# Kernel optimization log

Measured on AMD Instinct MI355X. Metric: run time of the kernel, lower is better.

Reference implementation:

```python
import jax, jax.numpy as jnp
import numpy as np

NUM_WIRES = 12
NUM_LAYERS = 3
BATCH = 8192
DIM = 2 ** NUM_WIRES


def _rx(theta):
    # RX(t) = [[cos(t/2), -i sin(t/2)], [-i sin(t/2), cos(t/2)]]; theta scalar or (B,)
    h = theta * 0.5
    c = jnp.cos(h).astype(jnp.complex64)
    s = (-1j) * jnp.sin(h).astype(jnp.complex64)
    return jnp.stack([jnp.stack([c, s], -1), jnp.stack([s, c], -1)], -2)


def _ry(theta):
    # RY(t) = [[cos(t/2), -sin(t/2)], [sin(t/2), cos(t/2)]]
    h = theta * 0.5
    c = jnp.cos(h)
    s = jnp.sin(h)
    m = jnp.stack([jnp.stack([c, -s], -1), jnp.stack([s, c], -1)], -2)
    return m.astype(jnp.complex64)


def _apply_1q(psi, mat, wire):
    # psi: (B, 2**n); pennylane wire 0 is most significant bit
    B = psi.shape[0]
    s = psi.reshape(B, 2 ** wire, 2, -1)
    if mat.ndim == 2:
        out = jnp.einsum('ij,bajc->baic', mat, s)
    else:  # per-sample gate, mat: (B, 2, 2)
        out = jnp.einsum('bij,bajc->baic', mat, s)
    return out.reshape(B, -1)


def _cnot(psi, control, target):
    B = psi.shape[0]
    a, b = (control, target) if control < target else (target, control)
    s = psi.reshape(B, 2 ** a, 2, 2 ** (b - a - 1), 2, -1)
    if control == a:
        # control on axis 2, flip target (axis 4) where control bit == 1
        s = s.at[:, :, 1].set(s[:, :, 1, :, ::-1])
    else:
        # control on axis 4, flip target (axis 2) where control bit == 1
        s = s.at[:, :, :, :, 1].set(s[:, :, ::-1, :, 1])
    return s.reshape(B, -1)


def _circuit(angles, weights):
    # angles: (B, n) per-sample input rotations; weights: (L, n, 2)
    B = angles.shape[0]
    n = NUM_WIRES
    psi = jnp.zeros((B, DIM), jnp.complex64).at[:, 0].set(1.0)
    for i in range(n):
        psi = _apply_1q(psi, _rx(angles[:, i]), i)
        psi = _apply_1q(psi, _ry(angles[:, i]), i)
    for l in range(NUM_LAYERS):
        for i in range(n):
            psi = _apply_1q(psi, _rx(weights[l, i, 0]), i)
            psi = _apply_1q(psi, _ry(weights[l, i, 1]), i)
        for i in range(n - 1):
            psi = _cnot(psi, i, i + 1)
        psi = _cnot(psi, n - 1, 0)
    probs = (psi.real ** 2 + psi.imag ** 2).reshape((B,) + (2,) * n)
    zs = []
    for i in range(n):
        other = tuple(j + 1 for j in range(n) if j != i)
        p = probs.sum(other)  # (B, 2)
        zs.append(p[:, 0] - p[:, 1])  # <Z_i> = P(0) - P(1)
    return jnp.stack(zs, -1)  # (B, n)


def setup_inputs() -> dict:
    key = jax.random.key(0)
    ks = jax.random.split(key, 5)
    return {
        'state_real': jax.random.normal(ks[0], (BATCH, DIM), jnp.float32),
        'state_imag': jax.random.normal(ks[1], (BATCH, DIM), jnp.float32),
        'weights': jax.random.normal(ks[2], (NUM_LAYERS, NUM_WIRES, 2), jnp.float32),
        'head_w': jax.random.normal(ks[3], (1, NUM_WIRES), jnp.float32) / np.sqrt(NUM_WIRES).astype(np.float32),
        'head_b': jax.random.normal(ks[4], (1,), jnp.float32),
    }


def reference(state_real, state_imag, weights, head_w, head_b):
    angles = jnp.arctan2(state_imag[:, :NUM_WIRES], state_real[:, :NUM_WIRES])  # (B, n)
    q = _circuit(angles, weights)  # (B, n)
    return (q @ head_w.T + head_b).squeeze(-1)  # (B,)
```

## Files before the change

### kernel.cpp

```cpp
#include <hip/hip_runtime.h>

typedef __fp16 h2v __attribute__((ext_vector_type(2)));
typedef _Float16 f16x8 __attribute__((ext_vector_type(8)));
typedef float f32x4 __attribute__((ext_vector_type(4)));

#define BLK 256
#define BATCH 8192

struct M12 { unsigned r[12]; };

constexpr M12 mp_matrix() {
  M12 m{};
  for (int p = 0; p <= 10; ++p) m.r[p] = (0xFFFu >> p) << p;
  m.r[11] = 0x7FFu;
  return m;
}
constexpr M12 MP = mp_matrix();

constexpr unsigned mv(const M12 m, unsigned v) {
  unsigned y = 0;
  for (int p = 0; p < 12; ++p)
    y |= (unsigned)(__builtin_popcount(m.r[p] & v) & 1) << p;
  return y;
}
constexpr M12 mmul(const M12 a, const M12 b) {
  M12 c{};
  for (int p = 0; p < 12; ++p) {
    unsigned acc = 0;
    for (int q = 0; q < 12; ++q)
      if ((a.r[p] >> q) & 1u) acc ^= b.r[q];
    c.r[p] = acc;
  }
  return c;
}
constexpr M12 minv(const M12 a0) {
  unsigned a[12] = {}, v[12] = {};
  for (int i = 0; i < 12; ++i) { a[i] = a0.r[i]; v[i] = 1u << i; }
  for (int c = 0; c < 12; ++c) {
    int piv = c;
    while (!((a[piv] >> c) & 1u)) ++piv;
    unsigned ta = a[piv], tv = v[piv];
    a[piv] = a[c]; v[piv] = v[c]; a[c] = ta; v[c] = tv;
    for (int r2 = 0; r2 < 12; ++r2)
      if (r2 != c && ((a[r2] >> c) & 1u)) { a[r2] ^= a[c]; v[r2] ^= v[c]; }
  }
  M12 out{};
  for (int i = 0; i < 12; ++i) out.r[i] = v[i];
  return out;
}
constexpr unsigned colq(const M12 m, int q) {
  unsigned c = 0;
  for (int p = 0; p < 12; ++p) c |= ((m.r[p] >> q) & 1u) << p;
  return c;
}
constexpr M12 from_cols(const unsigned (&c)[12]) {
  M12 m{};
  for (int p = 0; p < 12; ++p) {
    unsigned row = 0;
    for (int j = 0; j < 12; ++j) row |= ((c[j] >> p) & 1u) << j;
    m.r[p] = row;
  }
  return m;
}
constexpr M12 mk_id() { M12 m{}; for (int p = 0; p < 12; ++p) m.r[p] = 1u << p; return m; }
constexpr M12 MID = mk_id();
constexpr M12 MPI = minv(MP);

constexpr bool meq(const M12 a, const M12 b) {
  for (int p = 0; p < 12; ++p) if (a.r[p] != b.r[p]) return false;
  return true;
}
static_assert(meq(mmul(MP, MPI), MID), "P inverse");

struct Frame { M12 A, Ai; };
constexpr Frame FID{MID, MID};
constexpr Frame absorb(const Frame f) { return Frame{ mmul(MP, f.A), mmul(f.Ai, MPI) }; }
constexpr Frame apply_tau(const Frame f, const M12 t) {
  return Frame{ mmul(f.A, minv(t)), mmul(t, f.Ai) };
}

struct BSw { unsigned mk[7]; };
constexpr unsigned bswap(const BSw& b, unsigned v) {
  unsigned o = v;
  for (int k = 0; k < 7; ++k)
    if ((v >> (5 + k)) & 1u) o ^= b.mk[k];
  return o;
}
constexpr int rank5(const unsigned* v, int n) {
  unsigned basis[5] = {};
  int r = 0;
  for (int i = 0; i < n; ++i) {
    unsigned x = v[i];
    for (int b = 4; b >= 0; --b) {
      if (!((x >> b) & 1u)) continue;
      if (basis[b]) x ^= basis[b];
      else { basis[b] = x; ++r; break; }
    }
  }
  return r;
}
constexpr int readrank(const BSw& b) {
  unsigned v[5] = { bswap(b, 16u) & 0x1Cu, bswap(b, 32u) & 0x1Cu,
                    bswap(b, 64u) & 0x1Cu, bswap(b, 128u) & 0x1Cu,
                    bswap(b, 8u) & 0x1Cu };
  return rank5(v, 5);
}
constexpr int wrankf(const BSw& b, const unsigned* tv) {
  unsigned v[6] = {};
  for (int k = 0; k < 6; ++k) v[k] = bswap(b, tv[k]) & 0x1Fu;
  return rank5(v, 6);
}
constexpr BSw find_bsw(const M12 T, bool dpass) {
  unsigned src[6] = {16u, 32u, 64u, 128u, dpass ? 4u : 256u, dpass ? 8u : 512u};
  unsigned tv[6] = {};
  for (int k = 0; k < 6; ++k) tv[k] = mv(T, src[k]);
  BSw b{};
  b.mk[0] = 4u;
  int bw = wrankf(b, tv);
  for (int s = 0; s < 2; ++s)
    for (int k = 0; k < 7; ++k) {
      unsigned bestv = b.mk[k];
      for (unsigned v = 0; v < 8; ++v) {
        b.mk[k] = v << 2;
        if (readrank(b) < 3) continue;
        const int wr = wrankf(b, tv);
        if (wr > bw) { bw = wr; bestv = v << 2; }
      }
      b.mk[k] = bestv;
    }
  return b;
}

constexpr M12 mtw_c(const Frame f, const int* qs, const unsigned* tg, int c) {
  unsigned S[12] = {}, D[12] = {}, rows[4] = {};
  for (int i = 0; i < 4; ++i) {
    S[i] = colq(f.Ai, qs[i]);
    D[i] = tg[i];
    rows[i] = f.A.r[qs[i]];
  }
  unsigned R[4] = {rows[0], rows[1], rows[2], rows[3]};
  int pivcol[4] = {-1, -1, -1, -1};
  int nr = 0;
  for (int cc = 0; cc < 12 && nr < 4; ++cc) {
    int pr = -1;
    for (int r2 = nr; r2 < 4; ++r2) if ((R[r2] >> cc) & 1u) { pr = r2; break; }
    if (pr < 0) continue;
    unsigned tmp = R[nr]; R[nr] = R[pr]; R[pr] = tmp;
    for (int r2 = 0; r2 < 4; ++r2)
      if (r2 != nr && ((R[r2] >> cc) & 1u)) R[r2] ^= R[nr];
    pivcol[nr] = cc; ++nr;
  }
  unsigned nb[8] = {};
  int nc = 0;
  for (int j = 0; j < 12; ++j) {
    bool isp = false;
    for (int k = 0; k < nr; ++k) if (pivcol[k] == j) isp = true;
    if (isp) continue;
    unsigned v = 1u << j;
    for (int k = 0; k < nr; ++k) if ((R[k] >> j) & 1u) v |= 1u << pivcol[k];
    nb[nc] = v;
    ++nc;
  }
  for (int j = 0; j < 8; ++j) {
    S[4 + j] = nb[(j + c) & 7];
    D[4 + j] = 1u << (4 + j);
  }
  return mmul(from_cols(D), minv(from_cols(S)));
}
constexpr int tau_score(const M12 T, bool dpass) {
  const BSw b = find_bsw(T, dpass);
  unsigned src[6] = {16u, 32u, 64u, 128u, dpass ? 4u : 256u, dpass ? 8u : 512u};
  unsigned tv[6] = {};
  for (int k = 0; k < 6; ++k) tv[k] = mv(T, src[k]);
  return wrankf(b, tv);
}
constexpr M12 pick_tau(const Frame f, const int* qs, const unsigned* tg,
                       bool dpass) {
  int bc = 0, bs = -1;
  for (int c = 0; c < 8; ++c) {
    const M12 T = mtw_c(f, qs, tg, c);
    const int sc2 = tau_score(T, dpass);
    if (sc2 > bs) { bs = sc2; bc = c; }
  }
  return mtw_c(f, qs, tg, bc);
}
constexpr bool chk_group(const Frame f, const int* qs, const unsigned* tg) {
  for (int i = 0; i < 4; ++i) if (colq(f.Ai, qs[i]) != tg[i]) return false;
  return true;
}

constexpr int QA[4] = {11, 10, 9, 8};
constexpr int QB[4] = {7, 6, 5, 4};
constexpr int QC[4] = {3, 2, 1, 0};
constexpr unsigned T4[4] = {8u, 4u, 2u, 1u};

constexpr Frame F1  = absorb(FID);
constexpr M12  S2a = pick_tau(F1,  QA, T4, false);
constexpr Frame F2a = apply_tau(F1, S2a);
constexpr M12  S2b = pick_tau(F2a, QB, T4, true);
constexpr Frame F2b = apply_tau(F2a, S2b);
constexpr M12  S2c = pick_tau(F2b, QC, T4, true);
constexpr Frame F2c = apply_tau(F2b, S2c);
constexpr Frame F3  = absorb(F2c);
constexpr M12  S3a = pick_tau(F3,  QA, T4, true);
constexpr Frame F3a = apply_tau(F3, S3a);
constexpr M12  S3b = pick_tau(F3a, QB, T4, true);
constexpr Frame F3b = apply_tau(F3a, S3b);
constexpr M12  S3c = pick_tau(F3b, QC, T4, true);
constexpr Frame F3c = apply_tau(F3b, S3c);
constexpr Frame F4  = absorb(F3c);

static_assert(chk_group(F2a, QA, T4), "G2a");
static_assert(chk_group(F2b, QB, T4), "G2b");
static_assert(chk_group(F2c, QC, T4), "G2c");
static_assert(chk_group(F3a, QA, T4), "G3a");
static_assert(chk_group(F3b, QB, T4), "G3b");
static_assert(chk_group(F3c, QC, T4), "G3c");
static_assert(F2a.A.r[11] == 8u && F2a.A.r[10] == 4u && F2a.A.r[9] == 2u && F2a.A.r[8] == 1u, "rows2a");
static_assert(F2b.A.r[7]  == 8u && F2b.A.r[6]  == 4u && F2b.A.r[5] == 2u && F2b.A.r[4] == 1u, "rows2b");
static_assert(F2c.A.r[3]  == 8u && F2c.A.r[2]  == 4u && F2c.A.r[1] == 2u && F2c.A.r[0] == 1u, "rows2c");
static_assert(F3a.A.r[11] == 8u && F3a.A.r[10] == 4u && F3a.A.r[9] == 2u && F3a.A.r[8] == 1u, "rows3a");
static_assert(F3b.A.r[7]  == 8u && F3b.A.r[6]  == 4u && F3b.A.r[5] == 2u && F3b.A.r[4] == 1u, "rows3b");
static_assert(F3c.A.r[3]  == 8u && F3c.A.r[2]  == 4u && F3c.A.r[1] == 2u && F3c.A.r[0] == 1u, "rows3c");

constexpr BSw B0 = find_bsw(S2a, false);
constexpr BSw B1 = find_bsw(S2b, true);
constexpr BSw B2 = find_bsw(S2c, true);
constexpr BSw B3 = find_bsw(S3a, true);
constexpr BSw B4 = find_bsw(S3b, true);
constexpr BSw B5 = find_bsw(S3c, true);
static_assert(readrank(B0) == 3 && readrank(B1) == 3 && readrank(B2) == 3 &&
              readrank(B3) == 3 && readrank(B4) == 3 && readrank(B5) == 3, "rr");

struct PT {
  unsigned wc[16];
  unsigned wlb[6], wwb[2];
  unsigned rlb[5], rwb[2];
  unsigned rm[2];
};
constexpr PT mk_pt(const M12 T, const BSw b, bool dpass) {
  PT t{};
  for (int v = 0; v < 16; ++v) {
    const unsigned p = dpass ? ((((unsigned)v >> 2) << 8) | ((unsigned)v & 3u))
                             : (unsigned)v;
    t.wc[v] = bswap(b, mv(T, p));
  }
  unsigned src[6] = {16u, 32u, 64u, 128u, dpass ? 4u : 256u, dpass ? 8u : 512u};
  for (int k = 0; k < 6; ++k) t.wlb[k] = bswap(b, mv(T, src[k]));
  t.wwb[0] = bswap(b, mv(T, 1024u));
  t.wwb[1] = bswap(b, mv(T, 2048u));
  t.rlb[0] = bswap(b, 16u);  t.rlb[1] = bswap(b, 32u);
  t.rlb[2] = bswap(b, 64u);  t.rlb[3] = bswap(b, 128u);
  t.rlb[4] = bswap(b, 8u);
  t.rwb[0] = bswap(b, 1024u); t.rwb[1] = bswap(b, 2048u);
  t.rm[0] = bswap(b, 256u);   t.rm[1] = bswap(b, 512u);
  return t;
}
constexpr PT RT[6] = { mk_pt(S2a, B0, false), mk_pt(S2b, B1, true),
                       mk_pt(S2c, B2, true),  mk_pt(S3a, B3, true),
                       mk_pt(S3b, B4, true),  mk_pt(S3c, B5, true) };

template<int PI>
__device__ __forceinline__ unsigned wbase_of(const int lane, const int w) {
  unsigned wb = 0u;
  #pragma unroll
  for (int k = 0; k < 6; ++k) wb ^= ((lane >> k) & 1) ? RT[PI].wlb[k] : 0u;
  wb ^= (w & 1) ? RT[PI].wwb[0] : 0u;
  wb ^= (w & 2) ? RT[PI].wwb[1] : 0u;
  return wb;
}
template<int PI>
__device__ __forceinline__ unsigned rbase_of(const int lane, const int w) {
  unsigned rb = 0u;
  #pragma unroll
  for (int k = 0; k < 4; ++k) rb ^= ((lane >> k) & 1) ? RT[PI].rlb[k] : 0u;
  rb ^= ((lane >> 4) & 1) ? RT[PI].rlb[4] : 0u;
  rb ^= (w & 1) ? RT[PI].rwb[0] : 0u;
  rb ^= (w & 2) ? RT[PI].rwb[1] : 0u;
  return rb;
}

template<int PI>
__device__ __forceinline__ void do_pass(f32x4 (&D1)[4], f32x4 (&D2)[4],
                                        const unsigned* sb,
                                        const uint4 a1u, const uint4 a2u,
                                        const int lane, const int w,
                                        const unsigned sel) {
  const f16x8 A1f = __builtin_bit_cast(f16x8, a1u);
  const f16x8 A2f = __builtin_bit_cast(f16x8, a2u);
  const unsigned rb = rbase_of<PI>(lane, w);
  const f32x4 z4 = {0.f, 0.f, 0.f, 0.f};
  #pragma unroll
  for (int m = 0; m < 4; ++m) {
    const unsigned mo = rb ^ ((m & 1) ? RT[PI].rm[0] : 0u)
                           ^ ((m & 2) ? RT[PI].rm[1] : 0u);
    const uint4 lo = *(const uint4*)(sb + mo);
    const uint4 hi = *(const uint4*)(sb + (mo ^ 4u));
    uint4 bw;
    bw.x = __builtin_amdgcn_perm(lo.y, lo.x, sel);
    bw.y = __builtin_amdgcn_perm(lo.w, lo.z, sel);
    bw.z = __builtin_amdgcn_perm(hi.y, hi.x, sel);
    bw.w = __builtin_amdgcn_perm(hi.w, hi.z, sel);
    const f16x8 Bf = __builtin_bit_cast(f16x8, bw);
    D1[m] = __builtin_amdgcn_mfma_f32_16x16x32_f16(A1f, Bf, z4, 0, 0, 0);
    D2[m] = __builtin_amdgcn_mfma_f32_16x16x32_f16(A2f, Bf, z4, 0, 0, 0);
  }
}

template<int PI>
__device__ __forceinline__ void write_pass(const f32x4 (&D1)[4],
                                           const f32x4 (&D2)[4],
                                           unsigned* sb, const int lane,
                                           const int w) {
  const unsigned wb = wbase_of<PI>(lane, w);
  h2v* sh = (h2v*)sb;
  #pragma unroll
  for (int m = 0; m < 4; ++m)
    #pragma unroll
    for (int r = 0; r < 4; ++r)
      sh[wb ^ RT[PI].wc[(m << 2) | r]] =
          __builtin_amdgcn_cvt_pkrtz(D1[m][r], D2[m][r]);
}

__device__ __forceinline__ void gentry(const float4 g, const int rb,
                                       const int kb, float& re, float& im) {
  re = rb ? (kb ? g.x : g.z) : (kb ? -g.z : g.x);
  im = rb ? (kb ? -g.y : g.w) : (kb ? g.w : g.y);
}

__global__ __launch_bounds__(BLK) void amat_kernel(
    const float* __restrict__ wts, uint4* __restrict__ Am) {
  __shared__ float4 gt4[24];
  const int t = threadIdx.x;
  if (t < 24) {
    const int l = 1 + t / 12, i = t % 12;
    const float a  = wts[(l * 12 + i) * 2 + 0] * 0.5f;
    const float bb = wts[(l * 12 + i) * 2 + 1] * 0.5f;
    float sa, ca, sb2, cb;
    sincosf(a, &sa, &ca);
    sincosf(bb, &sb2, &cb);
    gt4[t] = make_float4(cb * ca, sb2 * sa, sb2 * ca, -cb * sa);
  }
  __syncthreads();
  #pragma unroll
  for (int rep = 0; rep < 3; ++rep) {
    const int idx = t + rep * BLK;
    const int pass = idx >> 7;
    const int mat  = (idx >> 6) & 1;
    const int lw   = idx & 63;
    const int r    = lw & 15;
    const int ks   = lw >> 4;
    const int imf  = ks >> 1;
    const float4 g0 = gt4[pass * 4 + 0];
    const float4 g1 = gt4[pass * 4 + 1];
    const float4 g2 = gt4[pass * 4 + 2];
    const float4 g3 = gt4[pass * 4 + 3];
    float b3r, b3i;
    gentry(g0, (r >> 3) & 1, ks & 1, b3r, b3i);
    float t2r[2], t2i[2];
    #pragma unroll
    for (int k2 = 0; k2 < 2; ++k2) {
      float cr, ci;
      gentry(g1, (r >> 2) & 1, k2, cr, ci);
      t2r[k2] = b3r * cr - b3i * ci;
      t2i[k2] = b3r * ci + b3i * cr;
    }
    float t1r[4], t1i[4];
    #pragma unroll
    for (int k2 = 0; k2 < 2; ++k2)
      #pragma unroll
      for (int k1 = 0; k1 < 2; ++k1) {
        float cr, ci;
        gentry(g2, (r >> 1) & 1, k1, cr, ci);
        t1r[k2 * 2 + k1] = t2r[k2] * cr - t2i[k2] * ci;
        t1i[k2 * 2 + k1] = t2r[k2] * ci + t2i[k2] * cr;
      }
    float ev[8];
    #pragma unroll
    for (int j = 0; j < 8; ++j) {
      float cr, ci;
      gentry(g3, r & 1, j & 1, cr, ci);
      const int h2 = j >> 1;
      const float er = t1r[h2] * cr - t1i[h2] * ci;
      const float ei = t1r[h2] * ci + t1i[h2] * cr;
      ev[j] = (mat == 0) ? (imf ? -ei : er) : (imf ? er : ei);
    }
    unsigned u[4];
    #pragma unroll
    for (int q = 0; q < 4; ++q) {
      const h2v pk = __builtin_amdgcn_cvt_pkrtz(ev[2 * q], ev[2 * q + 1]);
      u[q] = __builtin_bit_cast(unsigned, pk);
    }
    Am[(pass * 2 + mat) * 64 + lw] = make_uint4(u[0], u[1], u[2], u[3]);
  }
}

__global__ __launch_bounds__(BLK, 4) void qsim_kernel(
    const float* __restrict__ sr, const float* __restrict__ si,
    const float* __restrict__ wts, const float* __restrict__ hw,
    const float* __restrict__ hb, const uint4* __restrict__ Am,
    float* __restrict__ out) {
  __shared__ __align__(16) unsigned sbuf[2][4096];

  float4* qv = (float4*)(sbuf[1]);
  float* xacc = (float*)(sbuf[0]);

  const int t = threadIdx.x;
  const int lane = t & 63;
  const int w = t >> 6;
  const int s = blockIdx.x;

  uint4 A1u[6], A2u[6];
  #pragma unroll
  for (int p = 0; p < 6; ++p) {
    A1u[p] = Am[(p * 2 + 0) * 64 + lane];
    A2u[p] = Am[(p * 2 + 1) * 64 + lane];
  }

  if (t >= 64 && t < 76) {
    const int i = t - 64;
    const float ang = atan2f(si[(size_t)s * 4096 + i],
                             sr[(size_t)s * 4096 + i]) * 0.5f;
    float sn, cs;
    sincosf(ang, &sn, &cs);
    const float e0r = cs * cs, e0i = sn * sn, e1r = sn * cs, e1i = -sn * cs;
    const float a  = wts[i * 2 + 0] * 0.5f;
    const float bb = wts[i * 2 + 1] * 0.5f;
    float sa, ca, sb2, cb;
    sincosf(a, &sa, &ca);
    sincosf(bb, &sb2, &cb);
    const float g00r = cb * ca,  g00i = sb2 * sa, g01r = -sb2 * ca, g01i = -cb * sa;
    const float g10r = sb2 * ca, g10i = -cb * sa, g11r = cb * ca,   g11i = -sb2 * sa;
    const float q0r = g00r * e0r - g00i * e0i + g01r * e1r - g01i * e1i;
    const float q0i = g00r * e0i + g00i * e0r + g01r * e1i + g01i * e1r;
    const float q1r = g10r * e0r - g10i * e0i + g11r * e1r - g11i * e1i;
    const float q1i = g10r * e0i + g10i * e0r + g11r * e1i + g11i * e1r;
    qv[i] = make_float4(q0r, q0i, q1r, q1i);
  }
  __syncthreads();

  {
    const float4* q = qv;
    float Lr, Li;
    { const float4 q0 = q[0]; const int b0 = (w >> 1) & 1;
      Lr = b0 ? q0.z : q0.x; Li = b0 ? q0.w : q0.y; }
    { const float4 q1 = q[1]; const int b1 = w & 1;
      const float fr = b1 ? q1.z : q1.x, fi = b1 ? q1.w : q1.y;
      const float nr = Lr * fr - Li * fi, ni = Lr * fi + Li * fr;
      Lr = nr; Li = ni; }
    #pragma unroll
    for (int i = 2; i <= 7; ++i) {
      const float4 qq = q[i];
      const int bit = (lane >> (7 - i)) & 1;
      const float fr = bit ? qq.z : qq.x, fi = bit ? qq.w : qq.y;
      const float nr = Lr * fr - Li * fi, ni = Lr * fi + Li * fr;
      Lr = nr; Li = ni;
    }
    float LTr[4], LTi[4];
    { const float4 q8 = q[8], q9 = q[9];
      #pragma unroll
      for (int m = 0; m < 4; ++m) {
        const float xr2 = (m & 2) ? q8.z : q8.x, xi2 = (m & 2) ? q8.w : q8.y;
        const float yr = (m & 1) ? q9.z : q9.x, yi = (m & 1) ? q9.w : q9.y;
        const float tr = xr2 * yr - xi2 * yi, ti = xr2 * yi + xi2 * yr;
        LTr[m] = Lr * tr - Li * ti;
        LTi[m] = Lr * ti + Li * tr;
      } }
    float tbr[4], tbi[4];
    { const float4 qA = q[10], qB2 = q[11];
      #pragma unroll
      for (int m = 0; m < 4; ++m) {
        const float xr2 = (m & 2) ? qA.z : qA.x, xi2 = (m & 2) ? qA.w : qA.y;
        const float yr = (m & 1) ? qB2.z : qB2.x, yi = (m & 1) ? qB2.w : qB2.y;
        tbr[m] = xr2 * yr - xi2 * yi;
        tbi[m] = xr2 * yi + xi2 * yr;
      } }
    const unsigned wb = wbase_of<0>(lane, w);
    h2v* sh = (h2v*)sbuf[0];
    #pragma unroll
    for (int l = 0; l < 16; ++l) {
      const float arl = LTr[l >> 2] * tbr[l & 3] - LTi[l >> 2] * tbi[l & 3];
      const float ail = LTr[l >> 2] * tbi[l & 3] + LTi[l >> 2] * tbr[l & 3];
      sh[wb ^ RT[0].wc[l]] = __builtin_amdgcn_cvt_pkrtz(arl, ail);
    }
  }
  __syncthreads();

  const unsigned sel = (lane & 32) ? 0x07060302u : 0x05040100u;
  f32x4 D1[4], D2[4];

  do_pass<0>(D1, D2, sbuf[0], A1u[0], A2u[0], lane, w, sel);
  write_pass<1>(D1, D2, sbuf[1], lane, w);
  __syncthreads();
  do_pass<1>(D1, D2, sbuf[1], A1u[1], A2u[1], lane, w, sel);
  write_pass<2>(D1, D2, sbuf[0], lane, w);
  __syncthreads();
  do_pass<2>(D1, D2, sbuf[0], A1u[2], A2u[2], lane, w, sel);
  write_pass<3>(D1, D2, sbuf[1], lane, w);
  __syncthreads();
  do_pass<3>(D1, D2, sbuf[1], A1u[3], A2u[3], lane, w, sel);
  write_pass<4>(D1, D2, sbuf[0], lane, w);
  __syncthreads();
  do_pass<4>(D1, D2, sbuf[0], A1u[4], A2u[4], lane, w, sel);
  write_pass<5>(D1, D2, sbuf[1], lane, w);
  __syncthreads();
  do_pass<5>(D1, D2, sbuf[1], A1u[5], A2u[5], lane, w, sel);

  const unsigned pbase = ((unsigned)w << 10) | ((unsigned)(lane & 15) << 4) |
                         ((unsigned)((lane >> 4) & 3) << 2);
  float hp[12];
  #pragma unroll
  for (int i = 0; i < 12; ++i) {
    const unsigned R = F4.A.r[11 - i];
    const float h = hw[i];
    hp[i] = (__popc(pbase & R & 0xCFCu) & 1) ? -h : h;
  }
  float c[16];
  #pragma unroll
  for (int v = 0; v < 16; ++v) c[v] = 0.f;
  #pragma unroll
  for (int i = 0; i < 12; ++i) {
    const unsigned R = F4.A.r[11 - i];
    const int mu = (int)((((R >> 8) & 3u) << 2) | (R & 3u));
    c[mu] += hp[i];
  }
  #pragma unroll
  for (int bb = 1; bb < 16; bb <<= 1)
    #pragma unroll
    for (int v = 0; v < 16; ++v)
      if (!(v & bb)) {
        const float x = c[v], y = c[v | bb];
        c[v] = x + y;
        c[v | bb] = x - y;
      }
  float acc = 0.f;
  #pragma unroll
  for (int m = 0; m < 4; ++m)
    #pragma unroll
    for (int r = 0; r < 4; ++r)
      acc += (D1[m][r] * D1[m][r] + D2[m][r] * D2[m][r]) * c[(m << 2) | r];
  #pragma unroll
  for (int off = 1; off < 64; off <<= 1) acc += __shfl_xor(acc, off, 64);

  __syncthreads();
  if (lane == 0) xacc[w] = acc;
  __syncthreads();
  if (t == 0) out[s] = xacc[0] + xacc[1] + xacc[2] + xacc[3] + hb[0];
}

extern "C" void kernel_launch(void* const* d_in, const int* in_sizes, int n_in,
                              void* d_out, int out_size, void* d_ws, size_t ws_size,
                              hipStream_t stream) {
  const float* sr  = (const float*)d_in[0];
  const float* si  = (const float*)d_in[1];
  const float* wts = (const float*)d_in[2];
  const float* hw  = (const float*)d_in[3];
  const float* hb  = (const float*)d_in[4];
  float* out = (float*)d_out;
  uint4* Am = (uint4*)d_ws;
  amat_kernel<<<1, BLK, 0, stream>>>(wts, Am);
  qsim_kernel<<<BATCH, BLK, 0, stream>>>(sr, si, wts, hw, hb, Am, out);
}
```

Before: 103.2 us.

## Move permutation addressing from LDS writes to reads with linear vectorized stores

Replaces the per-pass write-side scatter (16 scalar h2v stores at swizzled addresses, chosen by a bank-swizzle search) with contiguous uint4 stores in a fixed linear layout. The basis change is instead folded into the read side: each pass gathers 8 scalar amplitudes via a precomputed offset table, with basis vectors picked greedily to keep read bank rank high. This cuts store instruction count and address math, but reads become 8 scalar LDS loads instead of two 128-bit loads, which may raise bank conflicts or latency. An extra __syncthreads is added before the initial state write.

```diff
diff --git a/kernel.cpp b/kernel.cpp
--- a/kernel.cpp
+++ b/kernel.cpp
@@ -79,18 +79,13 @@
   return Frame{ mmul(f.A, minv(t)), mmul(t, f.Ai) };
 }
 
-struct BSw { unsigned mk[7]; };
-constexpr unsigned bswap(const BSw& b, unsigned v) {
-  unsigned o = v;
-  for (int k = 0; k < 7; ++k)
-    if ((v >> (5 + k)) & 1u) o ^= b.mk[k];
-  return o;
-}
-constexpr int rank5(const unsigned* v, int n) {
+struct SSet { unsigned S[12]; };
+
+constexpr int bankrank(const unsigned* v, int n) {
   unsigned basis[5] = {};
   int r = 0;
   for (int i = 0; i < n; ++i) {
-    unsigned x = v[i];
+    unsigned x = v[i] & 31u;
     for (int b = 4; b >= 0; --b) {
       if (!((x >> b) & 1u)) continue;
       if (basis[b]) x ^= basis[b];
@@ -99,43 +94,19 @@
   }
   return r;
 }
-constexpr int readrank(const BSw& b) {
-  unsigned v[5] = { bswap(b, 16u) & 0x1Cu, bswap(b, 32u) & 0x1Cu,
-                    bswap(b, 64u) & 0x1Cu, bswap(b, 128u) & 0x1Cu,
-                    bswap(b, 8u) & 0x1Cu };
-  return rank5(v, 5);
-}
-constexpr int wrankf(const BSw& b, const unsigned* tv) {
-  unsigned v[6] = {};
-  for (int k = 0; k < 6; ++k) v[k] = bswap(b, tv[k]) & 0x1Fu;
-  return rank5(v, 6);
-}
-constexpr BSw find_bsw(const M12 T, bool dpass) {
-  unsigned src[6] = {16u, 32u, 64u, 128u, dpass ? 4u : 256u, dpass ? 8u : 512u};
-  unsigned tv[6] = {};
-  for (int k = 0; k < 6; ++k) tv[k] = mv(T, src[k]);
-  BSw b{};
-  b.mk[0] = 4u;
-  int bw = wrankf(b, tv);
-  for (int s = 0; s < 2; ++s)
-    for (int k = 0; k < 7; ++k) {
-      unsigned bestv = b.mk[k];
-      for (unsigned v = 0; v < 8; ++v) {
-        b.mk[k] = v << 2;
-        if (readrank(b) < 3) continue;
-        const int wr = wrankf(b, tv);
-        if (wr > bw) { bw = wr; bestv = v << 2; }
-      }
-      b.mk[k] = bestv;
-    }
-  return b;
-}
-
-constexpr M12 mtw_c(const Frame f, const int* qs, const unsigned* tg, int c) {
-  unsigned S[12] = {}, D[12] = {}, rows[4] = {};
+constexpr bool ins_ech(unsigned (&e)[12], unsigned x) {
+  for (int b = 11; b >= 0; --b) {
+    if (!((x >> b) & 1u)) continue;
+    if (e[b]) x ^= e[b];
+    else { e[b] = x; return true; }
+  }
+  return false;
+}
+constexpr SSet build_S(const Frame f, const int* qs) {
+  SSet s{};
+  unsigned rows[4] = {};
   for (int i = 0; i < 4; ++i) {
-    S[i] = colq(f.Ai, qs[i]);
-    D[i] = tg[i];
+    s.S[i] = colq(f.Ai, qs[i]);
     rows[i] = f.A.r[qs[i]];
   }
   unsigned R[4] = {rows[0], rows[1], rows[2], rows[3]};
@@ -161,114 +132,118 @@
     nb[nc] = v;
     ++nc;
   }
-  for (int j = 0; j < 8; ++j) {
-    S[4 + j] = nb[(j + c) & 7];
-    D[4 + j] = 1u << (4 + j);
-  }
-  return mmul(from_cols(D), minv(from_cols(S)));
-}
-constexpr int tau_score(const M12 T, bool dpass) {
-  const BSw b = find_bsw(T, dpass);
-  unsigned src[6] = {16u, 32u, 64u, 128u, dpass ? 4u : 256u, dpass ? 8u : 512u};
-  unsigned tv[6] = {};
-  for (int k = 0; k < 6; ++k) tv[k] = mv(T, src[k]);
-  return wrankf(b, tv);
-}
-constexpr M12 pick_tau(const Frame f, const int* qs, const unsigned* tg,
-                       bool dpass) {
-  int bc = 0, bs = -1;
-  for (int c = 0; c < 8; ++c) {
-    const M12 T = mtw_c(f, qs, tg, c);
-    const int sc2 = tau_score(T, dpass);
-    if (sc2 > bs) { bs = sc2; bc = c; }
-  }
-  return mtw_c(f, qs, tg, bc);
-}
-constexpr bool chk_group(const Frame f, const int* qs, const unsigned* tg) {
-  for (int i = 0; i < 4; ++i) if (colq(f.Ai, qs[i]) != tg[i]) return false;
+  unsigned pool[36] = {};
+  int np = 0;
+  for (int j = 0; j < 8; ++j) pool[np++] = nb[j];
+  for (int j = 0; j < 8; ++j)
+    for (int k = j + 1; k < 8; ++k) pool[np++] = nb[j] ^ nb[k];
+  unsigned ech[12] = {};
+  unsigned readset[5] = {};
+  int nrs = 0;
+  readset[nrs++] = s.S[0];
+  for (int slot = 4; slot <= 7; ++slot) {
+    int best = -1;
+    unsigned bestc = 0;
+    for (int c = 0; c < np; ++c) {
+      unsigned tmp[12];
+      for (int z = 0; z < 12; ++z) tmp[z] = ech[z];
+      if (!ins_ech(tmp, pool[c])) continue;
+      readset[nrs] = pool[c];
+      const int rk = bankrank(readset, nrs + 1);
+      if (rk > best) { best = rk; bestc = pool[c]; }
+    }
+    s.S[slot] = bestc;
+    ins_ech(ech, bestc);
+    readset[nrs++] = bestc;
+  }
+  const int rem[4] = {8, 9, 10, 11};
+  for (int t = 0; t < 4; ++t) {
+    for (int c = 0; c < np; ++c) {
+      unsigned tmp[12];
+      for (int z = 0; z < 12; ++z) tmp[z] = ech[z];
+      if (!ins_ech(tmp, pool[c])) continue;
+      s.S[rem[t]] = pool[c];
+      ins_ech(ech, pool[c]);
+      break;
+    }
+  }
+  return s;
+}
+constexpr unsigned T4[4] = {8u, 4u, 2u, 1u};
+constexpr M12 tau_of(const SSet s) {
+  unsigned Sc[12], Dc[12];
+  for (int i = 0; i < 12; ++i) {
+    Sc[i] = s.S[i];
+    Dc[i] = (i < 4) ? T4[i] : (1u << i);
+  }
+  return mmul(from_cols(Dc), minv(from_cols(Sc)));
+}
+constexpr int readrank_of(const SSet s) {
+  unsigned v[5] = {s.S[0], s.S[4], s.S[5], s.S[6], s.S[7]};
+  return bankrank(v, 5);
+}
+constexpr bool chk_group(const Frame f, const int* qs) {
+  for (int i = 0; i < 4; ++i) if (colq(f.Ai, qs[i]) != T4[i]) return false;
   return true;
 }
 
 constexpr int QA[4] = {11, 10, 9, 8};
 constexpr int QB[4] = {7, 6, 5, 4};
 constexpr int QC[4] = {3, 2, 1, 0};
-constexpr unsigned T4[4] = {8u, 4u, 2u, 1u};
 
 constexpr Frame F1  = absorb(FID);
-constexpr M12  S2a = pick_tau(F1,  QA, T4, false);
-constexpr Frame F2a = apply_tau(F1, S2a);
-constexpr M12  S2b = pick_tau(F2a, QB, T4, true);
-constexpr Frame F2b = apply_tau(F2a, S2b);
-constexpr M12  S2c = pick_tau(F2b, QC, T4, true);
-constexpr Frame F2c = apply_tau(F2b, S2c);
+constexpr SSet C0 = build_S(F1, QA);
+constexpr M12  T0 = tau_of(C0);
+constexpr Frame F2a = apply_tau(F1, T0);
+constexpr SSet C1 = build_S(F2a, QB);
+constexpr M12  T1 = tau_of(C1);
+constexpr Frame F2b = apply_tau(F2a, T1);
+constexpr SSet C2 = build_S(F2b, QC);
+constexpr M12  T2 = tau_of(C2);
+constexpr Frame F2c = apply_tau(F2b, T2);
 constexpr Frame F3  = absorb(F2c);
-constexpr M12  S3a = pick_tau(F3,  QA, T4, true);
-constexpr Frame F3a = apply_tau(F3, S3a);
-constexpr M12  S3b = pick_tau(F3a, QB, T4, true);
-constexpr Frame F3b = apply_tau(F3a, S3b);
-constexpr M12  S3c = pick_tau(F3b, QC, T4, true);
-constexpr Frame F3c = apply_tau(F3b, S3c);
+constexpr SSet C3 = build_S(F3, QA);
+constexpr M12  T3m = tau_of(C3);
+constexpr Frame F3a = apply_tau(F3, T3m);
+constexpr SSet C4 = build_S(F3a, QB);
+constexpr M12  T4m = tau_of(C4);
+constexpr Frame F3b = apply_tau(F3a, T4m);
+constexpr SSet C5 = build_S(F3b, QC);
+constexpr M12  T5m = tau_of(C5);
+constexpr Frame F3c = apply_tau(F3b, T5m);
 constexpr Frame F4  = absorb(F3c);
 
-static_assert(chk_group(F2a, QA, T4), "G2a");
-static_assert(chk_group(F2b, QB, T4), "G2b");
-static_assert(chk_group(F2c, QC, T4), "G2c");
-static_assert(chk_group(F3a, QA, T4), "G3a");
-static_assert(chk_group(F3b, QB, T4), "G3b");
-static_assert(chk_group(F3c, QC, T4), "G3c");
+static_assert(chk_group(F2a, QA), "G2a");
+static_assert(chk_group(F2b, QB), "G2b");
+static_assert(chk_group(F2c, QC), "G2c");
+static_assert(chk_group(F3a, QA), "G3a");
+static_assert(chk_group(F3b, QB), "G3b");
+static_assert(chk_group(F3c, QC), "G3c");
 static_assert(F2a.A.r[11] == 8u && F2a.A.r[10] == 4u && F2a.A.r[9] == 2u && F2a.A.r[8] == 1u, "rows2a");
 static_assert(F2b.A.r[7]  == 8u && F2b.A.r[6]  == 4u && F2b.A.r[5] == 2u && F2b.A.r[4] == 1u, "rows2b");
 static_assert(F2c.A.r[3]  == 8u && F2c.A.r[2]  == 4u && F2c.A.r[1] == 2u && F2c.A.r[0] == 1u, "rows2c");
 static_assert(F3a.A.r[11] == 8u && F3a.A.r[10] == 4u && F3a.A.r[9] == 2u && F3a.A.r[8] == 1u, "rows3a");
 static_assert(F3b.A.r[7]  == 8u && F3b.A.r[6]  == 4u && F3b.A.r[5] == 2u && F3b.A.r[4] == 1u, "rows3b");
 static_assert(F3c.A.r[3]  == 8u && F3c.A.r[2]  == 4u && F3c.A.r[1] == 2u && F3c.A.r[0] == 1u, "rows3c");
-
-constexpr BSw B0 = find_bsw(S2a, false);
-constexpr BSw B1 = find_bsw(S2b, true);
-constexpr BSw B2 = find_bsw(S2c, true);
-constexpr BSw B3 = find_bsw(S3a, true);
-constexpr BSw B4 = find_bsw(S3b, true);
-constexpr BSw B5 = find_bsw(S3c, true);
-static_assert(readrank(B0) == 3 && readrank(B1) == 3 && readrank(B2) == 3 &&
-              readrank(B3) == 3 && readrank(B4) == 3 && readrank(B5) == 3, "rr");
-
-struct PT {
-  unsigned wc[16];
-  unsigned wlb[6], wwb[2];
-  unsigned rlb[5], rwb[2];
-  unsigned rm[2];
-};
-constexpr PT mk_pt(const M12 T, const BSw b, bool dpass) {
+static_assert(readrank_of(C0) >= 3 && readrank_of(C1) >= 3 && readrank_of(C2) >= 3 &&
+              readrank_of(C3) >= 3 && readrank_of(C4) >= 3 && readrank_of(C5) >= 3, "rr");
+
+struct PT { unsigned rlb[5]; unsigned rwb[2]; unsigned ro[32]; };
+constexpr PT mk_pt(const SSet s) {
   PT t{};
-  for (int v = 0; v < 16; ++v) {
-    const unsigned p = dpass ? ((((unsigned)v >> 2) << 8) | ((unsigned)v & 3u))
-                             : (unsigned)v;
-    t.wc[v] = bswap(b, mv(T, p));
-  }
-  unsigned src[6] = {16u, 32u, 64u, 128u, dpass ? 4u : 256u, dpass ? 8u : 512u};
-  for (int k = 0; k < 6; ++k) t.wlb[k] = bswap(b, mv(T, src[k]));
-  t.wwb[0] = bswap(b, mv(T, 1024u));
-  t.wwb[1] = bswap(b, mv(T, 2048u));
-  t.rlb[0] = bswap(b, 16u);  t.rlb[1] = bswap(b, 32u);
-  t.rlb[2] = bswap(b, 64u);  t.rlb[3] = bswap(b, 128u);
-  t.rlb[4] = bswap(b, 8u);
-  t.rwb[0] = bswap(b, 1024u); t.rwb[1] = bswap(b, 2048u);
-  t.rm[0] = bswap(b, 256u);   t.rm[1] = bswap(b, 512u);
+  t.rlb[0] = s.S[4]; t.rlb[1] = s.S[5]; t.rlb[2] = s.S[6]; t.rlb[3] = s.S[7];
+  t.rlb[4] = s.S[0];
+  t.rwb[0] = s.S[10]; t.rwb[1] = s.S[11];
+  for (int m = 0; m < 4; ++m)
+    for (int j = 0; j < 8; ++j)
+      t.ro[(m << 3) | j] = ((m & 1) ? s.S[8] : 0u) ^ ((m & 2) ? s.S[9] : 0u) ^
+                           ((j & 1) ? s.S[3] : 0u) ^ ((j & 2) ? s.S[2] : 0u) ^
+                           ((j & 4) ? s.S[1] : 0u);
   return t;
 }
-constexpr PT RT[6] = { mk_pt(S2a, B0, false), mk_pt(S2b, B1, true),
-                       mk_pt(S2c, B2, true),  mk_pt(S3a, B3, true),
-                       mk_pt(S3b, B4, true),  mk_pt(S3c, B5, true) };
-
-template<int PI>
-__device__ __forceinline__ unsigned wbase_of(const int lane, const int w) {
-  unsigned wb = 0u;
-  #pragma unroll
-  for (int k = 0; k < 6; ++k) wb ^= ((lane >> k) & 1) ? RT[PI].wlb[k] : 0u;
-  wb ^= (w & 1) ? RT[PI].wwb[0] : 0u;
-  wb ^= (w & 2) ? RT[PI].wwb[1] : 0u;
-  return wb;
-}
+constexpr PT RT[6] = { mk_pt(C0), mk_pt(C1), mk_pt(C2),
+                       mk_pt(C3), mk_pt(C4), mk_pt(C5) };
+
 template<int PI>
 __device__ __forceinline__ unsigned rbase_of(const int lane, const int w) {
   unsigned rb = 0u;
@@ -292,34 +267,36 @@
   const f32x4 z4 = {0.f, 0.f, 0.f, 0.f};
   #pragma unroll
   for (int m = 0; m < 4; ++m) {
-    const unsigned mo = rb ^ ((m & 1) ? RT[PI].rm[0] : 0u)
-                           ^ ((m & 2) ? RT[PI].rm[1] : 0u);
-    const uint4 lo = *(const uint4*)(sb + mo);
-    const uint4 hi = *(const uint4*)(sb + (mo ^ 4u));
+    unsigned amp[8];
+    #pragma unroll
+    for (int j = 0; j < 8; ++j)
+      amp[j] = sb[rb ^ RT[PI].ro[(m << 3) | j]];
     uint4 bw;
-    bw.x = __builtin_amdgcn_perm(lo.y, lo.x, sel);
-    bw.y = __builtin_amdgcn_perm(lo.w, lo.z, sel);
-    bw.z = __builtin_amdgcn_perm(hi.y, hi.x, sel);
-    bw.w = __builtin_amdgcn_perm(hi.w, hi.z, sel);
+    bw.x = __builtin_amdgcn_perm(amp[1], amp[0], sel);
+    bw.y = __builtin_amdgcn_perm(amp[3], amp[2], sel);
+    bw.z = __builtin_amdgcn_perm(amp[5], amp[4], sel);
+    bw.w = __builtin_amdgcn_perm(amp[7], amp[6], sel);
     const f16x8 Bf = __builtin_bit_cast(f16x8, bw);
     D1[m] = __builtin_amdgcn_mfma_f32_16x16x32_f16(A1f, Bf, z4, 0, 0, 0);
     D2[m] = __builtin_amdgcn_mfma_f32_16x16x32_f16(A2f, Bf, z4, 0, 0, 0);
   }
 }
 
-template<int PI>
-__device__ __forceinline__ void write_pass(const f32x4 (&D1)[4],
-                                           const f32x4 (&D2)[4],
-                                           unsigned* sb, const int lane,
-                                           const int w) {
-  const unsigned wb = wbase_of<PI>(lane, w);
-  h2v* sh = (h2v*)sb;
-  #pragma unroll
-  for (int m = 0; m < 4; ++m)
-    #pragma unroll
-    for (int r = 0; r < 4; ++r)
-      sh[wb ^ RT[PI].wc[(m << 2) | r]] =
-          __builtin_amdgcn_cvt_pkrtz(D1[m][r], D2[m][r]);
+__device__ __forceinline__ void write_state(const f32x4 (&D1)[4],
+                                            const f32x4 (&D2)[4],
+                                            unsigned* sb, const int lane,
+                                            const int w) {
+  const unsigned base = ((unsigned)w << 10) | ((unsigned)(lane & 15) << 4) |
+                        ((unsigned)(lane >> 4) << 2);
+  #pragma unroll
+  for (int m = 0; m < 4; ++m) {
+    uint4 v;
+    v.x = __builtin_bit_cast(unsigned, __builtin_amdgcn_cvt_pkrtz(D1[m][0], D2[m][0]));
+    v.y = __builtin_bit_cast(unsigned, __builtin_amdgcn_cvt_pkrtz(D1[m][1], D2[m][1]));
+    v.z = __builtin_bit_cast(unsigned, __builtin_amdgcn_cvt_pkrtz(D1[m][2], D2[m][2]));
+    v.w = __builtin_bit_cast(unsigned, __builtin_amdgcn_cvt_pkrtz(D1[m][3], D2[m][3]));
+    *(uint4*)(sb + (base | ((unsigned)m << 8))) = v;
+  }
 }
 
 __device__ __forceinline__ void gentry(const float4 g, const int rb,
@@ -401,7 +378,6 @@
     const float* __restrict__ hb, const uint4* __restrict__ Am,
     float* __restrict__ out) {
   __shared__ __align__(16) unsigned sbuf[2][4096];
-
   float4* qv = (float4*)(sbuf[1]);
   float* xacc = (float*)(sbuf[0]);
 
@@ -475,13 +451,20 @@
         tbr[m] = xr2 * yr - xi2 * yi;
         tbi[m] = xr2 * yi + xi2 * yr;
       } }
-    const unsigned wb = wbase_of<0>(lane, w);
-    h2v* sh = (h2v*)sbuf[0];
-    #pragma unroll
-    for (int l = 0; l < 16; ++l) {
-      const float arl = LTr[l >> 2] * tbr[l & 3] - LTi[l >> 2] * tbi[l & 3];
-      const float ail = LTr[l >> 2] * tbi[l & 3] + LTi[l >> 2] * tbr[l & 3];
-      sh[wb ^ RT[0].wc[l]] = __builtin_amdgcn_cvt_pkrtz(arl, ail);
+    __syncthreads();
+    const unsigned base = ((unsigned)w << 10) | ((unsigned)lane << 4);
+    #pragma unroll
+    for (int qq2 = 0; qq2 < 4; ++qq2) {
+      uint4 v;
+      unsigned* vp = &v.x;
+      #pragma unroll
+      for (int z = 0; z < 4; ++z) {
+        const int l = qq2 * 4 + z;
+        const float arl = LTr[l >> 2] * tbr[l & 3] - LTi[l >> 2] * tbi[l & 3];
+        const float ail = LTr[l >> 2] * tbi[l & 3] + LTi[l >> 2] * tbr[l & 3];
+        vp[z] = __builtin_bit_cast(unsigned, __builtin_amdgcn_cvt_pkrtz(arl, ail));
+      }
+      *(uint4*)(sbuf[0] + base + qq2 * 4) = v;
     }
   }
   __syncthreads();
@@ -490,19 +473,19 @@
   f32x4 D1[4], D2[4];
 
   do_pass<0>(D1, D2, sbuf[0], A1u[0], A2u[0], lane, w, sel);
-  write_pass<1>(D1, D2, sbuf[1], lane, w);
+  write_state(D1, D2, sbuf[1], lane, w);
   __syncthreads();
   do_pass<1>(D1, D2, sbuf[1], A1u[1], A2u[1], lane, w, sel);
-  write_pass<2>(D1, D2, sbuf[0], lane, w);
+  write_state(D1, D2, sbuf[0], lane, w);
   __syncthreads();
   do_pass<2>(D1, D2, sbuf[0], A1u[2], A2u[2], lane, w, sel);
-  write_pass<3>(D1, D2, sbuf[1], lane, w);
+  write_state(D1, D2, sbuf[1], lane, w);
   __syncthreads();
   do_pass<3>(D1, D2, sbuf[1], A1u[3], A2u[3], lane, w, sel);
-  write_pass<4>(D1, D2, sbuf[0], lane, w);
+  write_state(D1, D2, sbuf[0], lane, w);
   __syncthreads();
   do_pass<4>(D1, D2, sbuf[0], A1u[4], A2u[4], lane, w, sel);
-  write_pass<5>(D1, D2, sbuf[1], lane, w);
+  write_state(D1, D2, sbuf[1], lane, w);
   __syncthreads();
   do_pass<5>(D1, D2, sbuf[1], A1u[5], A2u[5], lane, w, sel);
 
```

After: 103.3 us. About the same (+0.1%).
